# Optimization experiments

Hardware: AMD Instinct MI355X
Metric: run time of the kernel (lower is better)

The kernel has to match this reference:

```python
import jax, jax.numpy as jnp
import numpy as np

B, N_RES, N_ATOM, C_S, C_OUT = 2, 2048, 16384, 384, 50


def setup_inputs() -> dict:
    key = jax.random.key(0)
    k1, k2, k3 = jax.random.split(key, 3)
    # [B, n_res, c_s] single embedding
    s = jax.random.normal(k1, (B, N_RES, C_S), dtype=jnp.float32)
    # one-hot token->atom map: each atom selects exactly one residue
    atom_to_res = jax.random.randint(k2, (B, N_ATOM), 0, N_RES)
    token_to_atom_idx = jax.nn.one_hot(atom_to_res, N_RES, dtype=jnp.float32)  # [B, n_atom, n_res]
    # Linear(c_s, c_out) params (torch convention: W [c_out, c_s], b [c_out])
    W = jax.random.normal(k3, (C_OUT, C_S), dtype=jnp.float32) * 0.02
    b = jnp.zeros((C_OUT,), dtype=jnp.float32)
    return {"s": s, "token_to_atom_idx": token_to_atom_idx, "W": W, "b": b}


def reference(s, token_to_atom_idx, W, b):
    # sum_r one_hot[b,a,r] * s[b,r,c] -> broadcast-sum (a gather in disguise)
    atom_s = jnp.einsum('bar,brc->bac', token_to_atom_idx, s)  # [B, n_atom, c_s]
    logits = jnp.einsum('bac,oc->bao', atom_s, W) + b          # [B, n_atom, c_out]
    return logits
```

## Files before the change

kernel.cpp:

```cpp
#include <hip/hip_runtime.h>

#define B 2
#define N_RES 2048
#define N_ATOM 16384
#define C_S 384
#define C_OUT 50

__global__ __launch_bounds__(64) void proj_kernel(const float* __restrict__ s,
                                                  const float* __restrict__ W,
                                                  const float* __restrict__ bias,
                                                  float* __restrict__ proj) {
    int br = blockIdx.x;
    int lane = threadIdx.x;
    __shared__ float srow[C_S];
    const float* sp = s + (size_t)br * C_S;
    for (int i = lane; i < C_S; i += 64) srow[i] = sp[i];
    __syncthreads();
    if (lane < C_OUT) {
        const float* wp = W + lane * C_S;
        float acc = bias[lane];
        #pragma unroll 4
        for (int c = 0; c < C_S; c += 4) {
            float4 w4 = *(const float4*)(wp + c);
            acc += srow[c] * w4.x + srow[c + 1] * w4.y
                 + srow[c + 2] * w4.z + srow[c + 3] * w4.w;
        }
        proj[(size_t)br * C_OUT + lane] = acc;
    }
}

__global__ __launch_bounds__(256) void gather_kernel(const float* __restrict__ onehot,
                                                     const float* __restrict__ proj,
                                                     float* __restrict__ out) {
    int lane = threadIdx.x & 63;
    int w = (blockIdx.x << 2) + (threadIdx.x >> 6);
    const float* row = onehot + (size_t)w * N_RES;

    int r = 0;
    #pragma unroll 1
    for (int iter = 0; iter < N_RES / 256; ++iter) {
        int base = iter * 256 + lane * 4;
        float4 v = *(const float4*)(row + base);
        int j = -1;
        if (v.x != 0.f) j = 0;
        else if (v.y != 0.f) j = 1;
        else if (v.z != 0.f) j = 2;
        else if (v.w != 0.f) j = 3;
        unsigned long long mask = __ballot(j >= 0);
        if (mask) {
            int src = (int)__ffsll(mask) - 1;
            r = __shfl(base + j, src);
            break;
        }
    }

    int b = w >> 14;
    if (lane < C_OUT) {
        out[(size_t)w * C_OUT + lane] = proj[((size_t)b * N_RES + r) * C_OUT + lane];
    }
}

extern "C" void kernel_launch(void* const* d_in, const int* in_sizes, int n_in,
                              void* d_out, int out_size, void* d_ws, size_t ws_size,
                              hipStream_t stream) {
    const float* s      = (const float*)d_in[0];
    const float* onehot = (const float*)d_in[1];
    const float* W      = (const float*)d_in[2];
    const float* bias   = (const float*)d_in[3];
    float* out  = (float*)d_out;
    float* proj = (float*)d_ws;

    proj_kernel<<<B * N_RES, 64, 0, stream>>>(s, W, bias, proj);
    gather_kernel<<<(B * N_ATOM) / 4, 256, 0, stream>>>(onehot, proj, out);
}
```

Measured before the change: 383.0 us.

## Overlap one-hot index scan with projection in a fused kernel, gather via indices

Moves the one-hot row scan out of the gather kernel and into a fused kernel whose blocks either scan one-hot rows (writing an int index per atom) or compute the s·W projection. The memory-bound scan can then run concurrently with the projection instead of waiting behind it, and the scan loads are marked nontemporal. The gather kernel becomes a simple index lookup plus copy. This adds an extra index buffer round trip through global memory.

```diff
diff --git a/kernel.cpp b/kernel.cpp
--- a/kernel.cpp
+++ b/kernel.cpp
@@ -6,57 +6,72 @@
 #define C_S 384
 #define C_OUT 50
 
-__global__ __launch_bounds__(64) void proj_kernel(const float* __restrict__ s,
-                                                  const float* __restrict__ W,
-                                                  const float* __restrict__ bias,
-                                                  float* __restrict__ proj) {
-    int br = blockIdx.x;
-    int lane = threadIdx.x;
-    __shared__ float srow[C_S];
-    const float* sp = s + (size_t)br * C_S;
-    for (int i = lane; i < C_S; i += 64) srow[i] = sp[i];
-    __syncthreads();
-    if (lane < C_OUT) {
-        const float* wp = W + lane * C_S;
-        float acc = bias[lane];
-        #pragma unroll 4
-        for (int c = 0; c < C_S; c += 4) {
-            float4 w4 = *(const float4*)(wp + c);
-            acc += srow[c] * w4.x + srow[c + 1] * w4.y
-                 + srow[c + 2] * w4.z + srow[c + 3] * w4.w;
+#define SCAN_BLOCKS 8192
+#define PROJ_BLOCKS 1024
+
+typedef float nfloat4 __attribute__((ext_vector_type(4)));
+
+__global__ __launch_bounds__(256) void fused_scan_proj(const float* __restrict__ s,
+                                                       const float* __restrict__ W,
+                                                       const float* __restrict__ bias,
+                                                       const float* __restrict__ onehot,
+                                                       float* __restrict__ proj,
+                                                       int* __restrict__ idx) {
+    __shared__ float srow[4][C_S];
+    int wave = threadIdx.x >> 6;
+    int lane = threadIdx.x & 63;
+
+    if (blockIdx.x < SCAN_BLOCKS) {
+        int a = (blockIdx.x << 2) + wave;
+        const float* row = onehot + (size_t)a * N_RES;
+        int r = 0;
+        #pragma unroll 1
+        for (int iter = 0; iter < N_RES / 256; ++iter) {
+            int base = iter * 256 + (lane << 2);
+            nfloat4 v = __builtin_nontemporal_load((const nfloat4*)(row + base));
+            int j = -1;
+            if (v.x != 0.f) j = 0;
+            else if (v.y != 0.f) j = 1;
+            else if (v.z != 0.f) j = 2;
+            else if (v.w != 0.f) j = 3;
+            unsigned long long mask = __ballot(j >= 0);
+            if (mask) {
+                int src = (int)__ffsll(mask) - 1;
+                r = __shfl(base + j, src);
+                break;
+            }
         }
-        proj[(size_t)br * C_OUT + lane] = acc;
+        if (lane == 0) idx[a] = r;
+    } else {
+        int rr = ((blockIdx.x - SCAN_BLOCKS) << 2) + wave;
+        const float4* sp = (const float4*)(s + (size_t)rr * C_S);
+        float4* srp = (float4*)srow[wave];
+        for (int i = lane; i < C_S / 4; i += 64) srp[i] = sp[i];
+        __syncthreads();
+        if (lane < C_OUT) {
+            const float* wp = W + lane * C_S;
+            float acc = bias[lane];
+            #pragma unroll 4
+            for (int c = 0; c < C_S; c += 4) {
+                float4 w4 = *(const float4*)(wp + c);
+                acc += srow[wave][c]     * w4.x + srow[wave][c + 1] * w4.y
+                     + srow[wave][c + 2] * w4.z + srow[wave][c + 3] * w4.w;
+            }
+            proj[(size_t)rr * C_OUT + lane] = acc;
+        }
     }
 }
 
-__global__ __launch_bounds__(256) void gather_kernel(const float* __restrict__ onehot,
+__global__ __launch_bounds__(256) void gather_kernel(const int* __restrict__ idx,
                                                      const float* __restrict__ proj,
                                                      float* __restrict__ out) {
+    int wave = threadIdx.x >> 6;
     int lane = threadIdx.x & 63;
-    int w = (blockIdx.x << 2) + (threadIdx.x >> 6);
-    const float* row = onehot + (size_t)w * N_RES;
-
-    int r = 0;
-    #pragma unroll 1
-    for (int iter = 0; iter < N_RES / 256; ++iter) {
-        int base = iter * 256 + lane * 4;
-        float4 v = *(const float4*)(row + base);
-        int j = -1;
-        if (v.x != 0.f) j = 0;
-        else if (v.y != 0.f) j = 1;
-        else if (v.z != 0.f) j = 2;
-        else if (v.w != 0.f) j = 3;
-        unsigned long long mask = __ballot(j >= 0);
-        if (mask) {
-            int src = (int)__ffsll(mask) - 1;
-            r = __shfl(base + j, src);
-            break;
-        }
-    }
-
-    int b = w >> 14;
+    int a = (blockIdx.x << 2) + wave;
+    int r = idx[a];
+    int b = a >> 14;
     if (lane < C_OUT) {
-        out[(size_t)w * C_OUT + lane] = proj[((size_t)b * N_RES + r) * C_OUT + lane];
+        out[(size_t)a * C_OUT + lane] = proj[((size_t)b * N_RES + r) * C_OUT + lane];
     }
 }
 
@@ -68,8 +83,11 @@
     const float* W      = (const float*)d_in[2];
     const float* bias   = (const float*)d_in[3];
     float* out  = (float*)d_out;
+
     float* proj = (float*)d_ws;
+    int*   idx  = (int*)((char*)d_ws + (1 << 20));
 
-    proj_kernel<<<B * N_RES, 64, 0, stream>>>(s, W, bias, proj);
-    gather_kernel<<<(B * N_ATOM) / 4, 256, 0, stream>>>(onehot, proj, out);
+    fused_scan_proj<<<SCAN_BLOCKS + PROJ_BLOCKS, 256, 0, stream>>>(s, W, bias, onehot,
+                                                                   proj, idx);
+    gather_kernel<<<SCAN_BLOCKS, 256, 0, stream>>>(idx, proj, out);
 }
```

New measurement: 381.0 us. No clear change (-0.5%).
